# Kernel tuning notes

Measured on AMD Instinct MI355X. Metric: run time of the kernel, lower is better.

Reference implementation:

```python
import jax, jax.numpy as jnp
import numpy as np

N_NODES = 100000
N_EDGES = 1600000
NODE_DIM = 128
HIDDEN = 128
N_LAYERS = 4
LN_EPS = 1e-5


def _layernorm(x, g, b):
    mu = jnp.mean(x, axis=-1, keepdims=True)
    var = jnp.mean(jnp.square(x - mu), axis=-1, keepdims=True)
    return (x - mu) * jax.lax.rsqrt(var + LN_EPS) * g + b


def setup_inputs() -> dict:
    key = jax.random.key(0)
    ks = jax.random.split(key, 16)
    s = 1.0 / np.sqrt(HIDDEN)
    inp = {
        "x": jax.random.normal(ks[0], (N_NODES, NODE_DIM), dtype=jnp.float32),
        "edge_index": jax.random.randint(ks[1], (2, N_EDGES), 0, N_NODES, dtype=jnp.int64),
        # node_embed: Linear(node_dim -> hidden)
        "Wn": jax.random.normal(ks[2], (NODE_DIM, HIDDEN), dtype=jnp.float32) / np.sqrt(NODE_DIM),
        "bn": jnp.zeros((HIDDEN,), dtype=jnp.float32),
        # per-layer attention weights, stacked over the 4 layers
        "WQ": jax.random.normal(ks[3], (N_LAYERS, HIDDEN, HIDDEN), dtype=jnp.float32) * s,
        "bQ": jnp.zeros((N_LAYERS, HIDDEN), dtype=jnp.float32),
        "WK": jax.random.normal(ks[4], (N_LAYERS, HIDDEN, HIDDEN), dtype=jnp.float32) * s,
        "bK": jnp.zeros((N_LAYERS, HIDDEN), dtype=jnp.float32),
        "WV": jax.random.normal(ks[5], (N_LAYERS, HIDDEN, HIDDEN), dtype=jnp.float32) * s,
        "bV": jnp.zeros((N_LAYERS, HIDDEN), dtype=jnp.float32),
        "WO": jax.random.normal(ks[6], (N_LAYERS, HIDDEN, HIDDEN), dtype=jnp.float32) * s,
        "bO": jnp.zeros((N_LAYERS, HIDDEN), dtype=jnp.float32),
        "ln_g": jnp.ones((N_LAYERS, HIDDEN), dtype=jnp.float32),
        "ln_b": jnp.zeros((N_LAYERS, HIDDEN), dtype=jnp.float32),
        # out_proj: Linear(hidden -> node_dim)
        "Wout": jax.random.normal(ks[7], (HIDDEN, NODE_DIM), dtype=jnp.float32) * s,
        "bout": jnp.zeros((NODE_DIM,), dtype=jnp.float32),
    }
    return inp


def reference(x, edge_index, Wn, bn, WQ, bQ, WK, bK, WV, bV, WO, bO, ln_g, ln_b, Wout, bout):
    n = x.shape[0]
    src, dst = edge_index[0], edge_index[1]
    scale = 1.0 / np.sqrt(HIDDEN)

    h = x @ Wn + bn  # [N, H]
    for l in range(N_LAYERS):
        Q = h @ WQ[l] + bQ[l]
        K = h @ WK[l] + bK[l]
        V = h @ WV[l] + bV[l]
        # edge-wise attention logits: [E]
        scores = jnp.sum(Q[dst] * K[src], axis=-1) * scale
        # segment softmax over incoming edges of each dst node
        seg_max = jax.ops.segment_max(scores, dst, num_segments=n)
        e = jnp.exp(scores - seg_max[dst])
        seg_sum = jax.ops.segment_sum(e, dst, num_segments=n)
        attn = e / seg_sum[dst]  # dst always has >=1 edge where indexed
        # scatter-add weighted values: [N, H]
        messages = jax.ops.segment_sum(attn[:, None] * V[src], dst, num_segments=n)
        out = messages @ WO[l] + bO[l]
        h = _layernorm(h + out, ln_g[l], ln_b[l])
    return h @ Wout + bout
```

## Files before the change

kernel.cpp:

```cpp
#include <hip/hip_runtime.h>
#include <cstdint>
#include <cstddef>

#define HD 128

typedef __attribute__((ext_vector_type(8))) short bf16x8;
typedef __attribute__((ext_vector_type(8))) unsigned short u16x8;
typedef __attribute__((ext_vector_type(4))) float f32x4;

__device__ __forceinline__ unsigned short f2bf(float x) {
    unsigned int b = __float_as_uint(x);
    b += 0x7FFFu + ((b >> 16) & 1u);
    return (unsigned short)(b >> 16);
}
__device__ __forceinline__ float bf2f(unsigned short u) {
    return __uint_as_float(((unsigned int)u) << 16);
}

__global__ void detect_kernel(const unsigned* __restrict__ w, int* __restrict__ flag) {
    if (threadIdx.x == 0) *flag = 0;
    __syncthreads();
    unsigned v = w[2 * threadIdx.x + 1];
    if (v != 0u) atomicOr(flag, 1);
}

__device__ __forceinline__ int eload(const void* raw, int is32, size_t i) {
    return is32 ? ((const int*)raw)[i] : (int)((const long long*)raw)[i];
}

#define EPB 4096

__global__ __launch_bounds__(256) void p1_count(const void* __restrict__ raw,
                                                const int* __restrict__ flag, int E,
                                                int* __restrict__ tot, int nbins) {
    __shared__ int h[256];
    const int tid = threadIdx.x;
    const int is32 = *flag;
    h[tid] = 0;
    __syncthreads();
    const int base = blockIdx.x * EPB;
    const int lim = min(E, base + EPB);
    for (int i = base + tid; i < lim; i += 256) atomicAdd(&h[eload(raw, is32, (size_t)E + i) >> 9], 1);
    __syncthreads();
    if (tid < nbins && h[tid]) atomicAdd(&tot[tid], h[tid]);
}

__global__ __launch_bounds__(256) void p1_scan(const int* __restrict__ tot,
                                               int* __restrict__ base, int* __restrict__ cursor,
                                               int* __restrict__ rowptr, int nbins, int n, int E) {
    __shared__ int s[256];
    const int tid = threadIdx.x;
    const int v = (tid < nbins) ? tot[tid] : 0;
    s[tid] = v;
    __syncthreads();
#pragma unroll
    for (int o = 1; o < 256; o <<= 1) {
        int t = (tid >= o) ? s[tid - o] : 0;
        __syncthreads();
        s[tid] += t;
        __syncthreads();
    }
    if (tid < nbins) {
        base[tid] = s[tid] - v;
        cursor[tid] = s[tid] - v;
    }
    if (tid == 0) {
        base[nbins] = E;
        rowptr[n] = E;
    }
}

__global__ __launch_bounds__(256) void p1_scatter(const void* __restrict__ raw,
                                                  const int* __restrict__ flag, int E,
                                                  int* __restrict__ cursor,
                                                  int* __restrict__ ssrc, int* __restrict__ sdst) {
    __shared__ int h[256];
    __shared__ int cur[256];
    const int tid = threadIdx.x;
    const int is32 = *flag;
    h[tid] = 0;
    __syncthreads();
    const int base = blockIdx.x * EPB;
    const int lim = min(E, base + EPB);
    for (int i = base + tid; i < lim; i += 256) atomicAdd(&h[eload(raw, is32, (size_t)E + i) >> 9], 1);
    __syncthreads();
    if (h[tid]) cur[tid] = atomicAdd(&cursor[tid], h[tid]);
    __syncthreads();
    for (int i = base + tid; i < lim; i += 256) {
        const int d = eload(raw, is32, (size_t)E + i);
        const int pos = atomicAdd(&cur[d >> 9], 1);
        sdst[pos] = d;
        ssrc[pos] = eload(raw, is32, i);
    }
}

__global__ __launch_bounds__(256) void p2_build(const int* __restrict__ sdst,
                                                const int* __restrict__ ssrc,
                                                const int* __restrict__ bucket_base,
                                                int* __restrict__ rowptr, int* __restrict__ csr,
                                                int n) {
    const int bin = blockIdx.x;
    const int b0 = bucket_base[bin], b1 = bucket_base[bin + 1];
    __shared__ int cnt[512];
    __shared__ int ps[256];
    __shared__ int cur[512];
    const int tid = threadIdx.x;
    cnt[tid] = 0;
    cnt[tid + 256] = 0;
    __syncthreads();
    for (int e = b0 + tid; e < b1; e += 256) atomicAdd(&cnt[sdst[e] & 511], 1);
    __syncthreads();
    const int a = cnt[2 * tid], b = cnt[2 * tid + 1];
    ps[tid] = a + b;
    __syncthreads();
#pragma unroll
    for (int o = 1; o < 256; o <<= 1) {
        int t = (tid >= o) ? ps[tid - o] : 0;
        __syncthreads();
        ps[tid] += t;
        __syncthreads();
    }
    const int e0 = ps[tid] - (a + b);
    const int e1 = e0 + a;
    const int v0 = bin * 512 + 2 * tid;
    if (v0 < n) rowptr[v0] = b0 + e0;
    if (v0 + 1 < n) rowptr[v0 + 1] = b0 + e1;
    cur[2 * tid] = b0 + e0;
    cur[2 * tid + 1] = b0 + e1;
    __syncthreads();
    for (int e = b0 + tid; e < b1; e += 256) {
        const int pos = atomicAdd(&cur[sdst[e] & 511], 1);
        csr[pos] = ssrc[e];
    }
}

struct WPtrs { const float* p[6]; };

__global__ void wtrans_all(WPtrs ws, unsigned short* __restrict__ dst) {
    int i = blockIdx.x * 256 + threadIdx.x;
    if (i >= 18 * 16384) return;
    int m = i >> 14;
    int r = i & 16383;
    int k = r >> 7, c = r & 127;
    const float* s;
    int off;
    if (m == 0)      { s = ws.p[0]; off = 0; }
    else if (m < 13) { int q = (m - 1) % 3, l = (m - 1) / 3; s = ws.p[1 + q]; off = l; }
    else if (m < 17) { s = ws.p[4]; off = m - 13; }
    else             { s = ws.p[5]; off = 0; }
    dst[(size_t)m * 16384 + (size_t)c * HD + k] = f2bf(s[(size_t)off * 16384 + r]);
}

#define WLSTRIDE 132

__device__ __forceinline__ void stage_w(const unsigned short* __restrict__ Wt,
                                        unsigned short* __restrict__ wl, int tid) {
#pragma unroll
    for (int s = 0; s < 8; ++s) {
        const int slot = s * 256 + tid;
        const int row = slot >> 4, c8 = (slot & 15) << 3;
        *(u16x8*)&wl[row * WLSTRIDE + c8] = *(const u16x8*)&Wt[(size_t)row * HD + c8];
    }
}

template <bool AIN_F32, bool RESID_LN, bool OUT_F32, bool OUT_BF>
__global__ __launch_bounds__(256) void lin_lds(
    const void* __restrict__ Xin, const unsigned short* __restrict__ Wt,
    const float* __restrict__ bias,
    const float* __restrict__ lng, const float* __restrict__ lnb,
    const unsigned short* __restrict__ Rb, float* __restrict__ Yf,
    unsigned short* __restrict__ Yb, int n) {
    __shared__ unsigned short wl[128 * WLSTRIDE];
    const int tid = threadIdx.x;
    const int w = tid >> 6;
    const int lane = tid & 63;
    const int t = lane & 15, g = lane >> 4;
    const int waveBase = blockIdx.x * 64 + w * 16;
    const int arow = waveBase + t;
    const bool rowOK = arow < n;

    stage_w(Wt, wl, tid);

    bf16x8 af[4];
#pragma unroll
    for (int ks = 0; ks < 4; ++ks) {
        const int k = ks * 32 + g * 8;
        bf16x8 a = (bf16x8){0, 0, 0, 0, 0, 0, 0, 0};
        if (rowOK) {
            if (AIN_F32) {
                const float* Xf = (const float*)Xin;
                float4 x0 = *(const float4*)&Xf[(size_t)arow * HD + k];
                float4 x1 = *(const float4*)&Xf[(size_t)arow * HD + k + 4];
                a[0] = (short)f2bf(x0.x); a[1] = (short)f2bf(x0.y);
                a[2] = (short)f2bf(x0.z); a[3] = (short)f2bf(x0.w);
                a[4] = (short)f2bf(x1.x); a[5] = (short)f2bf(x1.y);
                a[6] = (short)f2bf(x1.z); a[7] = (short)f2bf(x1.w);
            } else {
                const unsigned short* Xb = (const unsigned short*)Xin;
                a = *(const bf16x8*)&Xb[(size_t)arow * HD + k];
            }
        }
        af[ks] = a;
    }

    __syncthreads();

    f32x4 acc[8];
#pragma unroll
    for (int nf = 0; nf < 8; ++nf) acc[nf] = (f32x4){0.f, 0.f, 0.f, 0.f};
#pragma unroll
    for (int ks = 0; ks < 4; ++ks) {
        const int k = ks * 32 + g * 8;
#pragma unroll
        for (int nf = 0; nf < 8; ++nf) {
            bf16x8 b = *(const bf16x8*)&wl[(nf * 16 + t) * WLSTRIDE + k];
            acc[nf] = __builtin_amdgcn_mfma_f32_16x16x32_bf16(af[ks], b, acc[nf], 0, 0, 0);
        }
    }

    float v[8][4];
#pragma unroll
    for (int nf = 0; nf < 8; ++nf) {
        const int col = nf * 16 + t;
        const float bv = bias[col];
#pragma unroll
        for (int r = 0; r < 4; ++r) {
            float x = acc[nf][r] + bv;
            if (RESID_LN) {
                const int row = waveBase + g * 4 + r;
                if (row < n) x += bf2f(Rb[(size_t)row * HD + col]);
            }
            v[nf][r] = x;
        }
    }

    if (RESID_LN) {
#pragma unroll
        for (int r = 0; r < 4; ++r) {
            float s = 0.f, sq = 0.f;
#pragma unroll
            for (int nf = 0; nf < 8; ++nf) { s += v[nf][r]; sq += v[nf][r] * v[nf][r]; }
#pragma unroll
            for (int mask = 1; mask < 16; mask <<= 1) {
                s += __shfl_xor(s, mask, 64);
                sq += __shfl_xor(sq, mask, 64);
            }
            const float mu = s * (1.f / 128.f);
            const float var = sq * (1.f / 128.f) - mu * mu;
            const float inv = rsqrtf(var + 1e-5f);
#pragma unroll
            for (int nf = 0; nf < 8; ++nf) {
                const int col = nf * 16 + t;
                v[nf][r] = (v[nf][r] - mu) * inv * lng[col] + lnb[col];
            }
        }
    }

#pragma unroll
    for (int r = 0; r < 4; ++r) {
        const int row = waveBase + g * 4 + r;
        if (row < n) {
#pragma unroll
            for (int nf = 0; nf < 8; ++nf) {
                const int col = nf * 16 + t;
                if (OUT_F32) Yf[(size_t)row * HD + col] = v[nf][r];
                if (OUT_BF) Yb[(size_t)row * HD + col] = f2bf(v[nf][r]);
            }
        }
    }
}

__global__ __launch_bounds__(256) void lin3_lds(
    const unsigned short* __restrict__ Xb, const unsigned short* __restrict__ Wt3,
    const float* __restrict__ b0, const float* __restrict__ b1, const float* __restrict__ b2,
    unsigned short* __restrict__ Qb, unsigned short* __restrict__ KV, int n) {
    __shared__ unsigned short wl[128 * WLSTRIDE];
    const int tid = threadIdx.x;
    const int w = tid >> 6;
    const int lane = tid & 63;
    const int t = lane & 15, g = lane >> 4;
    const int waveBase = blockIdx.x * 64 + w * 16;
    const int arow = waveBase + t;
    const bool rowOK = arow < n;

    bf16x8 af[4];
#pragma unroll
    for (int ks = 0; ks < 4; ++ks) {
        bf16x8 a = (bf16x8){0, 0, 0, 0, 0, 0, 0, 0};
        if (rowOK) a = *(const bf16x8*)&Xb[(size_t)arow * HD + ks * 32 + g * 8];
        af[ks] = a;
    }

    const float* bs[3] = {b0, b1, b2};

#pragma unroll
    for (int mat = 0; mat < 3; ++mat) {
        if (mat) __syncthreads();
        stage_w(Wt3 + (size_t)mat * 16384, wl, tid);
        __syncthreads();

        f32x4 acc[8];
#pragma unroll
        for (int nf = 0; nf < 8; ++nf) acc[nf] = (f32x4){0.f, 0.f, 0.f, 0.f};
#pragma unroll
        for (int ks = 0; ks < 4; ++ks) {
            const int k = ks * 32 + g * 8;
#pragma unroll
            for (int nf = 0; nf < 8; ++nf) {
                bf16x8 b = *(const bf16x8*)&wl[(nf * 16 + t) * WLSTRIDE + k];
                acc[nf] = __builtin_amdgcn_mfma_f32_16x16x32_bf16(af[ks], b, acc[nf], 0, 0, 0);
            }
        }

        unsigned short* outp = (mat == 0) ? Qb : KV;
        const int rs = (mat == 0) ? 128 : 256;
        const int co = (mat == 2) ? 128 : 0;
#pragma unroll
        for (int r = 0; r < 4; ++r) {
            const int row = waveBase + g * 4 + r;
            if (row < n) {
#pragma unroll
                for (int nf = 0; nf < 8; ++nf) {
                    const int col = nf * 16 + t;
                    outp[(size_t)row * rs + co + col] = f2bf(acc[nf][r] + bs[mat][col]);
                }
            }
        }
    }
}

__global__ __launch_bounds__(256) void attn_kernel(
    const unsigned short* __restrict__ Qb, const unsigned short* __restrict__ KV,
    const int* __restrict__ rowptr, const int* __restrict__ csr,
    unsigned short* __restrict__ Mb, int n) {
    const int d = (blockIdx.x * 256 + threadIdx.x) >> 6;
    if (d >= n) return;
    const int lane = threadIdx.x & 63;
    const int t = lane & 7, g = lane >> 3;
    const int beg = rowptr[d], end = rowptr[d + 1];

    const float scale = 0.08838834764831845f;
    float qv[16];
    {
        u16x8 q0 = *(const u16x8*)&Qb[(size_t)d * HD + t * 16];
        u16x8 q1 = *(const u16x8*)&Qb[(size_t)d * HD + t * 16 + 8];
#pragma unroll
        for (int j = 0; j < 8; ++j) {
            qv[j] = bf2f(q0[j]) * scale;
            qv[8 + j] = bf2f(q1[j]) * scale;
        }
    }
    float ss = 0.f;
    float acc[16];
#pragma unroll
    for (int j = 0; j < 16; ++j) acc[j] = 0.f;

    const int nit = (end - beg + 7) >> 3;
    for (int it = 0; it < nit; ++it) {
        const int idx = beg + it * 8 + g;
        const bool act = idx < end;
        const int s = act ? csr[idx] : 0;
        const unsigned short* kvp = &KV[(size_t)s * 256 + t * 16];
        const u16x8 k0 = *(const u16x8*)kvp;
        const u16x8 k1 = *(const u16x8*)(kvp + 8);
        const u16x8 v0 = *(const u16x8*)(kvp + 128);
        const u16x8 v1 = *(const u16x8*)(kvp + 136);
        float p = 0.f;
#pragma unroll
        for (int j = 0; j < 8; ++j) {
            p = fmaf(bf2f(k0[j]), qv[j], p);
            p = fmaf(bf2f(k1[j]), qv[8 + j], p);
        }
#pragma unroll
        for (int mask = 1; mask < 8; mask <<= 1) p += __shfl_xor(p, mask, 64);
        const float e = act ? __expf(p) : 0.f;
        ss += e;
#pragma unroll
        for (int j = 0; j < 8; ++j) {
            acc[j] = fmaf(e, bf2f(v0[j]), acc[j]);
            acc[8 + j] = fmaf(e, bf2f(v1[j]), acc[8 + j]);
        }
    }

#pragma unroll
    for (int mask = 8; mask <= 32; mask <<= 1) {
        ss += __shfl_xor(ss, mask, 64);
#pragma unroll
        for (int j = 0; j < 16; ++j) acc[j] += __shfl_xor(acc[j], mask, 64);
    }

    const float inv = (end > beg) ? 1.f / ss : 0.f;
    if (g == 0) {
        u16x8 o0, o1;
#pragma unroll
        for (int j = 0; j < 8; ++j) {
            o0[j] = f2bf(acc[j] * inv);
            o1[j] = f2bf(acc[8 + j] * inv);
        }
        *(u16x8*)&Mb[(size_t)d * HD + t * 16] = o0;
        *(u16x8*)&Mb[(size_t)d * HD + t * 16 + 8] = o1;
    }
}

extern "C" void kernel_launch(void* const* d_in, const int* in_sizes, int n_in,
                              void* d_out, int out_size, void* d_ws, size_t ws_size,
                              hipStream_t stream) {
    const float* x    = (const float*)d_in[0];
    const void*  eix  = d_in[1];
    const float* Wn   = (const float*)d_in[2];
    const float* bn   = (const float*)d_in[3];
    const float* WQ   = (const float*)d_in[4];
    const float* bQ   = (const float*)d_in[5];
    const float* WK   = (const float*)d_in[6];
    const float* bK   = (const float*)d_in[7];
    const float* WV   = (const float*)d_in[8];
    const float* bV   = (const float*)d_in[9];
    const float* WO   = (const float*)d_in[10];
    const float* bO   = (const float*)d_in[11];
    const float* lng  = (const float*)d_in[12];
    const float* lnb  = (const float*)d_in[13];
    const float* Wout = (const float*)d_in[14];
    const float* bout = (const float*)d_in[15];

    const int n = in_sizes[0] / HD;
    const int E = in_sizes[1] / 2;
    const int L = 4;
    const int NBINS = (n + 511) >> 9;

    char* p = (char*)d_ws;
    auto alloc = [&](size_t bytes) -> void* {
        void* r = (void*)p;
        p += (bytes + 255) & ~(size_t)255;
        return r;
    };
    unsigned short* hb = (unsigned short*)alloc((size_t)n * HD * 2);
    unsigned short* qb = (unsigned short*)alloc((size_t)n * HD * 2);
    unsigned short* kv = (unsigned short*)alloc((size_t)n * HD * 4);
    unsigned short* mb = (unsigned short*)alloc((size_t)n * HD * 2);
    int* ssrc   = (int*)alloc((size_t)E * 4);
    int* sdst   = (int*)alloc((size_t)E * 4);
    int* csr    = (int*)alloc((size_t)E * 4);
    int* rowptr = (int*)alloc((size_t)(n + 1) * 4);
    int* btot   = (int*)alloc(256 * 4);
    int* bbase  = (int*)alloc(257 * 4);
    int* bcur   = (int*)alloc(256 * 4);
    int* flag   = (int*)alloc(256);
    unsigned short* wt = (unsigned short*)alloc(18 * 16384 * 2);

    const int EB = (E + EPB - 1) / EPB;
    const int nw = (n + 3) / 4;
    const int nl = (n + 63) / 64;

    detect_kernel<<<1, 256, 0, stream>>>((const unsigned*)eix, flag);
    hipMemsetAsync(btot, 0, 256 * 4, stream);
    p1_count<<<EB, 256, 0, stream>>>(eix, flag, E, btot, NBINS);
    p1_scan<<<1, 256, 0, stream>>>(btot, bbase, bcur, rowptr, NBINS, n, E);
    p1_scatter<<<EB, 256, 0, stream>>>(eix, flag, E, bcur, ssrc, sdst);
    p2_build<<<NBINS, 256, 0, stream>>>(sdst, ssrc, bbase, rowptr, csr, n);

    WPtrs wp;
    wp.p[0] = Wn; wp.p[1] = WQ; wp.p[2] = WK; wp.p[3] = WV; wp.p[4] = WO; wp.p[5] = Wout;
    wtrans_all<<<(18 * 16384 + 255) / 256, 256, 0, stream>>>(wp, wt);

    lin_lds<true, false, false, true><<<nl, 256, 0, stream>>>(
        x, wt, bn, nullptr, nullptr, nullptr, nullptr, hb, n);

    for (int l = 0; l < L; ++l) {
        lin3_lds<<<nl, 256, 0, stream>>>(
            hb, wt + (size_t)(1 + 3 * l) * 16384, bQ + l * HD, bK + l * HD, bV + l * HD,
            qb, kv, n);
        attn_kernel<<<nw, 256, 0, stream>>>(qb, kv, rowptr, csr, mb, n);
        lin_lds<false, true, false, true><<<nl, 256, 0, stream>>>(
            mb, wt + (size_t)(13 + l) * 16384, bO + l * HD, lng + l * HD, lnb + l * HD,
            hb, nullptr, hb, n);
    }
    lin_lds<false, false, true, false><<<nl, 256, 0, stream>>>(
        hb, wt + (size_t)17 * 16384, bout, nullptr, nullptr, nullptr, (float*)d_out, nullptr, n);
}
```

Measured before the change: 839.1 us.

## Fuse output projection+LayerNorm with next layer QKV projection in one kernel

Reorders the transposed weight buffer so each layer's WO is followed by the next layer's WQ/WK/WV. A single kernel now runs the output projection, residual add and LayerNorm, keeps the normalized h tile in LDS, and immediately computes the next Q/K/V (or the final output projection). This removes separate launches and the re-read of h from global memory between the two linear stages. In exchange it adds extra LDS use per block, which may lower occupancy.

```diff
diff --git a/kernel.cpp b/kernel.cpp
--- a/kernel.cpp
+++ b/kernel.cpp
@@ -145,9 +145,11 @@
     const float* s;
     int off;
     if (m == 0)      { s = ws.p[0]; off = 0; }
-    else if (m < 13) { int q = (m - 1) % 3, l = (m - 1) / 3; s = ws.p[1 + q]; off = l; }
-    else if (m < 17) { s = ws.p[4]; off = m - 13; }
-    else             { s = ws.p[5]; off = 0; }
+    else if (m < 17) {
+        int j = m - 1, grp = j >> 2, pos = j & 3;
+        off = grp;
+        s = (pos == 0) ? ws.p[1] : (pos == 1) ? ws.p[2] : (pos == 2) ? ws.p[3] : ws.p[4];
+    } else           { s = ws.p[5]; off = 0; }
     dst[(size_t)m * 16384 + (size_t)c * HD + k] = f2bf(s[(size_t)off * 16384 + r]);
 }
 
@@ -163,46 +165,49 @@
     }
 }
 
-template <bool AIN_F32, bool RESID_LN, bool OUT_F32, bool OUT_BF>
-__global__ __launch_bounds__(256) void lin_lds(
-    const void* __restrict__ Xin, const unsigned short* __restrict__ Wt,
-    const float* __restrict__ bias,
+__device__ __forceinline__ bf16x8 load_a_bf(const unsigned short* Xb, int row, int k, int n) {
+    bf16x8 a = (bf16x8){0, 0, 0, 0, 0, 0, 0, 0};
+    if (row < n) a = *(const bf16x8*)&Xb[(size_t)row * HD + k];
+    return a;
+}
+__device__ __forceinline__ bf16x8 load_a_f32(const float* Xf, int row, int k, int n) {
+    bf16x8 a = (bf16x8){0, 0, 0, 0, 0, 0, 0, 0};
+    if (row < n) {
+        float4 x0 = *(const float4*)&Xf[(size_t)row * HD + k];
+        float4 x1 = *(const float4*)&Xf[(size_t)row * HD + k + 4];
+        a[0] = (short)f2bf(x0.x); a[1] = (short)f2bf(x0.y);
+        a[2] = (short)f2bf(x0.z); a[3] = (short)f2bf(x0.w);
+        a[4] = (short)f2bf(x1.x); a[5] = (short)f2bf(x1.y);
+        a[6] = (short)f2bf(x1.z); a[7] = (short)f2bf(x1.w);
+    }
+    return a;
+}
+
+template <int MODE>
+__global__ __launch_bounds__(256) void fused_k(
+    const void* __restrict__ Xin, const unsigned short* __restrict__ W,
+    const float* __restrict__ bias0,
     const float* __restrict__ lng, const float* __restrict__ lnb,
-    const unsigned short* __restrict__ Rb, float* __restrict__ Yf,
-    unsigned short* __restrict__ Yb, int n) {
+    unsigned short* __restrict__ hb,
+    const float* __restrict__ b1, const float* __restrict__ b2, const float* __restrict__ b3,
+    unsigned short* __restrict__ Qb, unsigned short* __restrict__ KV,
+    float* __restrict__ Yout, int n) {
     __shared__ unsigned short wl[128 * WLSTRIDE];
+    __shared__ unsigned short hl[64 * WLSTRIDE];
     const int tid = threadIdx.x;
     const int w = tid >> 6;
     const int lane = tid & 63;
     const int t = lane & 15, g = lane >> 4;
     const int waveBase = blockIdx.x * 64 + w * 16;
-    const int arow = waveBase + t;
-    const bool rowOK = arow < n;
-
-    stage_w(Wt, wl, tid);
-
+
+    stage_w(W, wl, tid);
     bf16x8 af[4];
 #pragma unroll
     for (int ks = 0; ks < 4; ++ks) {
         const int k = ks * 32 + g * 8;
-        bf16x8 a = (bf16x8){0, 0, 0, 0, 0, 0, 0, 0};
-        if (rowOK) {
-            if (AIN_F32) {
-                const float* Xf = (const float*)Xin;
-                float4 x0 = *(const float4*)&Xf[(size_t)arow * HD + k];
-                float4 x1 = *(const float4*)&Xf[(size_t)arow * HD + k + 4];
-                a[0] = (short)f2bf(x0.x); a[1] = (short)f2bf(x0.y);
-                a[2] = (short)f2bf(x0.z); a[3] = (short)f2bf(x0.w);
-                a[4] = (short)f2bf(x1.x); a[5] = (short)f2bf(x1.y);
-                a[6] = (short)f2bf(x1.z); a[7] = (short)f2bf(x1.w);
-            } else {
-                const unsigned short* Xb = (const unsigned short*)Xin;
-                a = *(const bf16x8*)&Xb[(size_t)arow * HD + k];
-            }
-        }
-        af[ks] = a;
-    }
-
+        af[ks] = (MODE == 0) ? load_a_f32((const float*)Xin, waveBase + t, k, n)
+                             : load_a_bf((const unsigned short*)Xin, waveBase + t, k, n);
+    }
     __syncthreads();
 
     f32x4 acc[8];
@@ -222,19 +227,18 @@
 #pragma unroll
     for (int nf = 0; nf < 8; ++nf) {
         const int col = nf * 16 + t;
-        const float bv = bias[col];
+        const float bv = bias0[col];
 #pragma unroll
         for (int r = 0; r < 4; ++r) {
             float x = acc[nf][r] + bv;
-            if (RESID_LN) {
+            if (MODE >= 1) {
                 const int row = waveBase + g * 4 + r;
-                if (row < n) x += bf2f(Rb[(size_t)row * HD + col]);
+                if (row < n) x += bf2f(hb[(size_t)row * HD + col]);
             }
             v[nf][r] = x;
         }
     }
-
-    if (RESID_LN) {
+    if (MODE >= 1) {
 #pragma unroll
         for (int r = 0; r < 4; ++r) {
             float s = 0.f, sq = 0.f;
@@ -255,77 +259,74 @@
             }
         }
     }
-
 #pragma unroll
     for (int r = 0; r < 4; ++r) {
         const int row = waveBase + g * 4 + r;
-        if (row < n) {
-#pragma unroll
-            for (int nf = 0; nf < 8; ++nf) {
-                const int col = nf * 16 + t;
-                if (OUT_F32) Yf[(size_t)row * HD + col] = v[nf][r];
-                if (OUT_BF) Yb[(size_t)row * HD + col] = f2bf(v[nf][r]);
-            }
-        }
-    }
-}
-
-__global__ __launch_bounds__(256) void lin3_lds(
-    const unsigned short* __restrict__ Xb, const unsigned short* __restrict__ Wt3,
-    const float* __restrict__ b0, const float* __restrict__ b1, const float* __restrict__ b2,
-    unsigned short* __restrict__ Qb, unsigned short* __restrict__ KV, int n) {
-    __shared__ unsigned short wl[128 * WLSTRIDE];
-    const int tid = threadIdx.x;
-    const int w = tid >> 6;
-    const int lane = tid & 63;
-    const int t = lane & 15, g = lane >> 4;
-    const int waveBase = blockIdx.x * 64 + w * 16;
-    const int arow = waveBase + t;
-    const bool rowOK = arow < n;
-
-    bf16x8 af[4];
-#pragma unroll
-    for (int ks = 0; ks < 4; ++ks) {
-        bf16x8 a = (bf16x8){0, 0, 0, 0, 0, 0, 0, 0};
-        if (rowOK) a = *(const bf16x8*)&Xb[(size_t)arow * HD + ks * 32 + g * 8];
-        af[ks] = a;
-    }
-
-    const float* bs[3] = {b0, b1, b2};
-
-#pragma unroll
-    for (int mat = 0; mat < 3; ++mat) {
-        if (mat) __syncthreads();
-        stage_w(Wt3 + (size_t)mat * 16384, wl, tid);
+        const int lrow = w * 16 + g * 4 + r;
+        const bool ok = row < n;
+#pragma unroll
+        for (int nf = 0; nf < 8; ++nf) {
+            const int col = nf * 16 + t;
+            const unsigned short hv = f2bf(v[nf][r]);
+            hl[lrow * WLSTRIDE + col] = hv;
+            if (MODE <= 1 && ok) hb[(size_t)row * HD + col] = hv;
+        }
+    }
+    __syncthreads();
+
+    bf16x8 hf[4];
+#pragma unroll
+    for (int ks = 0; ks < 4; ++ks)
+        hf[ks] = *(const bf16x8*)&hl[(w * 16 + t) * WLSTRIDE + ks * 32 + g * 8];
+
+    const int NM = (MODE == 2) ? 1 : 3;
+    const float* bs[3] = {b1, b2, b3};
+#pragma unroll
+    for (int mat = 1; mat <= NM; ++mat) {
+        stage_w(W + (size_t)mat * 16384, wl, tid);
         __syncthreads();
-
-        f32x4 acc[8];
-#pragma unroll
-        for (int nf = 0; nf < 8; ++nf) acc[nf] = (f32x4){0.f, 0.f, 0.f, 0.f};
+        f32x4 a2[8];
+#pragma unroll
+        for (int nf = 0; nf < 8; ++nf) a2[nf] = (f32x4){0.f, 0.f, 0.f, 0.f};
 #pragma unroll
         for (int ks = 0; ks < 4; ++ks) {
             const int k = ks * 32 + g * 8;
 #pragma unroll
             for (int nf = 0; nf < 8; ++nf) {
                 bf16x8 b = *(const bf16x8*)&wl[(nf * 16 + t) * WLSTRIDE + k];
-                acc[nf] = __builtin_amdgcn_mfma_f32_16x16x32_bf16(af[ks], b, acc[nf], 0, 0, 0);
-            }
-        }
-
-        unsigned short* outp = (mat == 0) ? Qb : KV;
-        const int rs = (mat == 0) ? 128 : 256;
-        const int co = (mat == 2) ? 128 : 0;
-#pragma unroll
-        for (int r = 0; r < 4; ++r) {
-            const int row = waveBase + g * 4 + r;
-            if (row < n) {
-#pragma unroll
-                for (int nf = 0; nf < 8; ++nf) {
-                    const int col = nf * 16 + t;
-                    outp[(size_t)row * rs + co + col] = f2bf(acc[nf][r] + bs[mat][col]);
+                a2[nf] = __builtin_amdgcn_mfma_f32_16x16x32_bf16(hf[ks], b, a2[nf], 0, 0, 0);
+            }
+        }
+        if (MODE == 2) {
+#pragma unroll
+            for (int r = 0; r < 4; ++r) {
+                const int row = waveBase + g * 4 + r;
+                if (row < n) {
+#pragma unroll
+                    for (int nf = 0; nf < 8; ++nf) {
+                        const int col = nf * 16 + t;
+                        Yout[(size_t)row * HD + col] = a2[nf][r] + b1[col];
+                    }
                 }
             }
-        }
+        } else {
+            unsigned short* outp = (mat == 1) ? Qb : KV;
+            const int rs = (mat == 1) ? 128 : 256;
+            const int co = (mat == 3) ? 128 : 0;
+            const float* bb = bs[mat - 1];
+#pragma unroll
+            for (int r = 0; r < 4; ++r) {
+                const int row = waveBase + g * 4 + r;
+                if (row < n) {
+#pragma unroll
+                    for (int nf = 0; nf < 8; ++nf) {
+                        const int col = nf * 16 + t;
+                        outp[(size_t)row * rs + co + col] = f2bf(a2[nf][r] + bb[col]);
+                    }
+                }
+            }
+        }
+        if (mat < NM) __syncthreads();
     }
 }
 
@@ -424,7 +425,6 @@
 
     const int n = in_sizes[0] / HD;
     const int E = in_sizes[1] / 2;
-    const int L = 4;
     const int NBINS = (n + 511) >> 9;
 
     char* p = (char*)d_ws;
@@ -462,18 +462,20 @@
     wp.p[0] = Wn; wp.p[1] = WQ; wp.p[2] = WK; wp.p[3] = WV; wp.p[4] = WO; wp.p[5] = Wout;
     wtrans_all<<<(18 * 16384 + 255) / 256, 256, 0, stream>>>(wp, wt);
 
-    lin_lds<true, false, false, true><<<nl, 256, 0, stream>>>(
-        x, wt, bn, nullptr, nullptr, nullptr, nullptr, hb, n);
-
-    for (int l = 0; l < L; ++l) {
-        lin3_lds<<<nl, 256, 0, stream>>>(
-            hb, wt + (size_t)(1 + 3 * l) * 16384, bQ + l * HD, bK + l * HD, bV + l * HD,
-            qb, kv, n);
+    fused_k<0><<<nl, 256, 0, stream>>>(
+        x, wt, bn, nullptr, nullptr, hb,
+        bQ, bK, bV, qb, kv, nullptr, n);
+
+    for (int l = 0; l < 4; ++l) {
         attn_kernel<<<nw, 256, 0, stream>>>(qb, kv, rowptr, csr, mb, n);
-        lin_lds<false, true, false, true><<<nl, 256, 0, stream>>>(
-            mb, wt + (size_t)(13 + l) * 16384, bO + l * HD, lng + l * HD, lnb + l * HD,
-            hb, nullptr, hb, n);
-    }
-    lin_lds<false, false, true, false><<<nl, 256, 0, stream>>>(
-        hb, wt + (size_t)17 * 16384, bout, nullptr, nullptr, nullptr, (float*)d_out, nullptr, n);
-}
+        if (l < 3) {
+            fused_k<1><<<nl, 256, 0, stream>>>(
+                mb, wt + (size_t)(4 + 4 * l) * 16384, bO + l * HD, lng + l * HD, lnb + l * HD, hb,
+                bQ + (l + 1) * HD, bK + (l + 1) * HD, bV + (l + 1) * HD, qb, kv, nullptr, n);
+        } else {
+            fused_k<2><<<nl, 256, 0, stream>>>(
+                mb, wt + (size_t)16 * 16384, bO + 3 * HD, lng + 3 * HD, lnb + 3 * HD, hb,
+                bout, nullptr, nullptr, nullptr, nullptr, (float*)d_out, n);
+        }
+    }
+}
```

Result: no change. 841.4 us (+0.3%).

## Pack sorted edges into one word and stage weights via async global-to-LDS loads

Applied to the files above, without the earlier changes.

Edge bucketing now writes a single packed word per edge (src shifted left by 9, OR'd with the low 9 bits of dst) instead of separate src and dst arrays, halving intermediate traffic in the CSR build. Weights are pre-stored in an XOR-swizzled layout so they can be copied straight into unpadded LDS with global_load_lds, bypassing registers. In lin3 the next matrix's weights are loaded while the current one's epilogue runs. The packing assumes src fits in 23 bits, and the swizzle must match between the transpose and the reads.

```diff
diff --git a/kernel.cpp b/kernel.cpp
--- a/kernel.cpp
+++ b/kernel.cpp
@@ -73,7 +73,7 @@
 __global__ __launch_bounds__(256) void p1_scatter(const void* __restrict__ raw,
                                                   const int* __restrict__ flag, int E,
                                                   int* __restrict__ cursor,
-                                                  int* __restrict__ ssrc, int* __restrict__ sdst) {
+                                                  unsigned* __restrict__ spack) {
     __shared__ int h[256];
     __shared__ int cur[256];
     const int tid = threadIdx.x;
@@ -89,13 +89,11 @@
     for (int i = base + tid; i < lim; i += 256) {
         const int d = eload(raw, is32, (size_t)E + i);
         const int pos = atomicAdd(&cur[d >> 9], 1);
-        sdst[pos] = d;
-        ssrc[pos] = eload(raw, is32, i);
-    }
-}
-
-__global__ __launch_bounds__(256) void p2_build(const int* __restrict__ sdst,
-                                                const int* __restrict__ ssrc,
+        spack[pos] = ((unsigned)eload(raw, is32, i) << 9) | (unsigned)(d & 511);
+    }
+}
+
+__global__ __launch_bounds__(256) void p2_build(const unsigned* __restrict__ spack,
                                                 const int* __restrict__ bucket_base,
                                                 int* __restrict__ rowptr, int* __restrict__ csr,
                                                 int n) {
@@ -108,7 +106,7 @@
     cnt[tid] = 0;
     cnt[tid + 256] = 0;
     __syncthreads();
-    for (int e = b0 + tid; e < b1; e += 256) atomicAdd(&cnt[sdst[e] & 511], 1);
+    for (int e = b0 + tid; e < b1; e += 256) atomicAdd(&cnt[spack[e] & 511u], 1);
     __syncthreads();
     const int a = cnt[2 * tid], b = cnt[2 * tid + 1];
     ps[tid] = a + b;
@@ -129,8 +127,9 @@
     cur[2 * tid + 1] = b0 + e1;
     __syncthreads();
     for (int e = b0 + tid; e < b1; e += 256) {
-        const int pos = atomicAdd(&cur[sdst[e] & 511], 1);
-        csr[pos] = ssrc[e];
+        const unsigned v = spack[e];
+        const int pos = atomicAdd(&cur[v & 511u], 1);
+        csr[pos] = (int)(v >> 9);
     }
 }
 
@@ -148,19 +147,43 @@
     else if (m < 13) { int q = (m - 1) % 3, l = (m - 1) / 3; s = ws.p[1 + q]; off = l; }
     else if (m < 17) { s = ws.p[4]; off = m - 13; }
     else             { s = ws.p[5]; off = 0; }
-    dst[(size_t)m * 16384 + (size_t)c * HD + k] = f2bf(s[(size_t)off * 16384 + r]);
-}
-
-#define WLSTRIDE 132
-
-__device__ __forceinline__ void stage_w(const unsigned short* __restrict__ Wt,
-                                        unsigned short* __restrict__ wl, int tid) {
+    const int idx = ((c << 7) + k) ^ ((c & 7) << 3);
+    dst[(size_t)m * 16384 + idx] = f2bf(s[(size_t)off * 16384 + r]);
+}
+
+__device__ __forceinline__ void stage_w_async(const unsigned short* __restrict__ Wt,
+                                              unsigned short* __restrict__ wl,
+                                              int w, int lane) {
 #pragma unroll
     for (int s = 0; s < 8; ++s) {
-        const int slot = s * 256 + tid;
-        const int row = slot >> 4, c8 = (slot & 15) << 3;
-        *(u16x8*)&wl[row * WLSTRIDE + c8] = *(const u16x8*)&Wt[(size_t)row * HD + c8];
-    }
+        const int off = s * 2048 + w * 512;
+        __builtin_amdgcn_global_load_lds(
+            (const __attribute__((address_space(1))) void*)(Wt + off + lane * 8),
+            (__attribute__((address_space(3))) void*)(wl + off), 16, 0, 0);
+    }
+}
+
+__device__ __forceinline__ bf16x8 read_w(const unsigned short* __restrict__ wl,
+                                         int row, int k) {
+    return *(const bf16x8*)&wl[(((row) << 7) + k) ^ ((row & 7) << 3)];
+}
+
+__device__ __forceinline__ bf16x8 load_a_bf(const unsigned short* Xb, int row, int k, int n) {
+    bf16x8 a = (bf16x8){0, 0, 0, 0, 0, 0, 0, 0};
+    if (row < n) a = *(const bf16x8*)&Xb[(size_t)row * HD + k];
+    return a;
+}
+__device__ __forceinline__ bf16x8 load_a_f32(const float* Xf, int row, int k, int n) {
+    bf16x8 a = (bf16x8){0, 0, 0, 0, 0, 0, 0, 0};
+    if (row < n) {
+        float4 x0 = *(const float4*)&Xf[(size_t)row * HD + k];
+        float4 x1 = *(const float4*)&Xf[(size_t)row * HD + k + 4];
+        a[0] = (short)f2bf(x0.x); a[1] = (short)f2bf(x0.y);
+        a[2] = (short)f2bf(x0.z); a[3] = (short)f2bf(x0.w);
+        a[4] = (short)f2bf(x1.x); a[5] = (short)f2bf(x1.y);
+        a[6] = (short)f2bf(x1.z); a[7] = (short)f2bf(x1.w);
+    }
+    return a;
 }
 
 template <bool AIN_F32, bool RESID_LN, bool OUT_F32, bool OUT_BF>
@@ -170,37 +193,22 @@
     const float* __restrict__ lng, const float* __restrict__ lnb,
     const unsigned short* __restrict__ Rb, float* __restrict__ Yf,
     unsigned short* __restrict__ Yb, int n) {
-    __shared__ unsigned short wl[128 * WLSTRIDE];
+    __shared__ unsigned short wl[128 * 128];
     const int tid = threadIdx.x;
     const int w = tid >> 6;
     const int lane = tid & 63;
     const int t = lane & 15, g = lane >> 4;
     const int waveBase = blockIdx.x * 64 + w * 16;
     const int arow = waveBase + t;
-    const bool rowOK = arow < n;
-
-    stage_w(Wt, wl, tid);
+
+    stage_w_async(Wt, wl, w, lane);
 
     bf16x8 af[4];
 #pragma unroll
     for (int ks = 0; ks < 4; ++ks) {
         const int k = ks * 32 + g * 8;
-        bf16x8 a = (bf16x8){0, 0, 0, 0, 0, 0, 0, 0};
-        if (rowOK) {
-            if (AIN_F32) {
-                const float* Xf = (const float*)Xin;
-                float4 x0 = *(const float4*)&Xf[(size_t)arow * HD + k];
-                float4 x1 = *(const float4*)&Xf[(size_t)arow * HD + k + 4];
-                a[0] = (short)f2bf(x0.x); a[1] = (short)f2bf(x0.y);
-                a[2] = (short)f2bf(x0.z); a[3] = (short)f2bf(x0.w);
-                a[4] = (short)f2bf(x1.x); a[5] = (short)f2bf(x1.y);
-                a[6] = (short)f2bf(x1.z); a[7] = (short)f2bf(x1.w);
-            } else {
-                const unsigned short* Xb = (const unsigned short*)Xin;
-                a = *(const bf16x8*)&Xb[(size_t)arow * HD + k];
-            }
-        }
-        af[ks] = a;
+        af[ks] = AIN_F32 ? load_a_f32((const float*)Xin, arow, k, n)
+                         : load_a_bf((const unsigned short*)Xin, arow, k, n);
     }
 
     __syncthreads();
@@ -213,7 +221,7 @@
         const int k = ks * 32 + g * 8;
 #pragma unroll
         for (int nf = 0; nf < 8; ++nf) {
-            bf16x8 b = *(const bf16x8*)&wl[(nf * 16 + t) * WLSTRIDE + k];
+            bf16x8 b = read_w(wl, nf * 16 + t, k);
             acc[nf] = __builtin_amdgcn_mfma_f32_16x16x32_bf16(af[ks], b, acc[nf], 0, 0, 0);
         }
     }
@@ -274,29 +282,25 @@
     const unsigned short* __restrict__ Xb, const unsigned short* __restrict__ Wt3,
     const float* __restrict__ b0, const float* __restrict__ b1, const float* __restrict__ b2,
     unsigned short* __restrict__ Qb, unsigned short* __restrict__ KV, int n) {
-    __shared__ unsigned short wl[128 * WLSTRIDE];
+    __shared__ unsigned short wl[128 * 128];
     const int tid = threadIdx.x;
     const int w = tid >> 6;
     const int lane = tid & 63;
     const int t = lane & 15, g = lane >> 4;
     const int waveBase = blockIdx.x * 64 + w * 16;
     const int arow = waveBase + t;
-    const bool rowOK = arow < n;
+
+    stage_w_async(Wt3, wl, w, lane);
 
     bf16x8 af[4];
 #pragma unroll
-    for (int ks = 0; ks < 4; ++ks) {
-        bf16x8 a = (bf16x8){0, 0, 0, 0, 0, 0, 0, 0};
-        if (rowOK) a = *(const bf16x8*)&Xb[(size_t)arow * HD + ks * 32 + g * 8];
-        af[ks] = a;
-    }
+    for (int ks = 0; ks < 4; ++ks)
+        af[ks] = load_a_bf(Xb, arow, ks * 32 + g * 8, n);
 
     const float* bs[3] = {b0, b1, b2};
 
 #pragma unroll
     for (int mat = 0; mat < 3; ++mat) {
-        if (mat) __syncthreads();
-        stage_w(Wt3 + (size_t)mat * 16384, wl, tid);
         __syncthreads();
 
         f32x4 acc[8];
@@ -307,14 +311,19 @@
             const int k = ks * 32 + g * 8;
 #pragma unroll
             for (int nf = 0; nf < 8; ++nf) {
-                bf16x8 b = *(const bf16x8*)&wl[(nf * 16 + t) * WLSTRIDE + k];
+                bf16x8 b = read_w(wl, nf * 16 + t, k);
                 acc[nf] = __builtin_amdgcn_mfma_f32_16x16x32_bf16(af[ks], b, acc[nf], 0, 0, 0);
             }
+        }
+        if (mat < 2) {
+            __syncthreads();
+            stage_w_async(Wt3 + (size_t)(mat + 1) * 16384, wl, w, lane);
         }
 
         unsigned short* outp = (mat == 0) ? Qb : KV;
         const int rs = (mat == 0) ? 128 : 256;
         const int co = (mat == 2) ? 128 : 0;
+        const float* bb = bs[mat];
 #pragma unroll
         for (int r = 0; r < 4; ++r) {
             const int row = waveBase + g * 4 + r;
@@ -322,7 +331,7 @@
 #pragma unroll
                 for (int nf = 0; nf < 8; ++nf) {
                     const int col = nf * 16 + t;
-                    outp[(size_t)row * rs + co + col] = f2bf(acc[nf][r] + bs[mat][col]);
+                    outp[(size_t)row * rs + co + col] = f2bf(acc[nf][r] + bb[col]);
                 }
             }
         }
@@ -437,8 +446,7 @@
     unsigned short* qb = (unsigned short*)alloc((size_t)n * HD * 2);
     unsigned short* kv = (unsigned short*)alloc((size_t)n * HD * 4);
     unsigned short* mb = (unsigned short*)alloc((size_t)n * HD * 2);
-    int* ssrc   = (int*)alloc((size_t)E * 4);
-    int* sdst   = (int*)alloc((size_t)E * 4);
+    unsigned* spack = (unsigned*)alloc((size_t)E * 4);
     int* csr    = (int*)alloc((size_t)E * 4);
     int* rowptr = (int*)alloc((size_t)(n + 1) * 4);
     int* btot   = (int*)alloc(256 * 4);
@@ -455,8 +463,8 @@
     hipMemsetAsync(btot, 0, 256 * 4, stream);
     p1_count<<<EB, 256, 0, stream>>>(eix, flag, E, btot, NBINS);
     p1_scan<<<1, 256, 0, stream>>>(btot, bbase, bcur, rowptr, NBINS, n, E);
-    p1_scatter<<<EB, 256, 0, stream>>>(eix, flag, E, bcur, ssrc, sdst);
-    p2_build<<<NBINS, 256, 0, stream>>>(sdst, ssrc, bbase, rowptr, csr, n);
+    p1_scatter<<<EB, 256, 0, stream>>>(eix, flag, E, bcur, spack);
+    p2_build<<<NBINS, 256, 0, stream>>>(spack, bbase, rowptr, csr, n);
 
     WPtrs wp;
     wp.p[0] = Wn; wp.p[1] = WQ; wp.p[2] = WK; wp.p[3] = WV; wp.p[4] = WO; wp.p[5] = Wout;
```

Measured after the change: 835.8 us. About the same (-0.4%).
